# Kernel tuning notes

Hardware: AMD Instinct MI355X
Metric: run time of the kernel (lower is better)

## Reference

```python
import jax, jax.numpy as jnp
import numpy as np


def conv2d(x, w, pad, groups=1):
    # x: [B,Cin,H,W], w: [Cout,Cin/groups,K,K]
    return jax.lax.conv_general_dilated(
        x, w, (1, 1), [(pad, pad), (pad, pad)],
        dimension_numbers=('NCHW', 'OIHW', 'NCHW'),
        feature_group_count=groups)


def setup_inputs() -> dict:
    key = jax.random.key(0)
    ks = jax.random.split(key, 24)
    B, C, H, W = 16, 512, 32, 128          # batch, encoder_dim, feature map
    Da, Ds, De, Dm = 512, 256, 256, 1024   # att_dim, state_dim, embed_dim, mem_dim
    V, Dmerge = 1000, 512
    K, P = 11, 5
    Din = De + C + Dm                       # GRU input dim = 1792
    s = 0.02
    rn = lambda k, shp, sc=1.0: jax.random.normal(k, shp, jnp.float32) * sc
    return {
        'encode': rn(ks[0], (B, C, H, W)),
        'encode_pro': rn(ks[1], (B, Da, H, W)),
        'encode_mask': jnp.ones((B, 1, H, W), jnp.float32),
        'state': rn(ks[2], (B, Ds)),
        'pre_weight': jax.random.uniform(ks[3], (B, 1, H, W), jnp.float32),
        'cum_weight': jax.random.uniform(ks[4], (B, 1, H, W), jnp.float32),
        'context': rn(ks[5], (B, C)),
        'cond_mem': rn(ks[6], (B, Dm)),
        'cond_weight': jax.random.uniform(ks[7], (B, 2, H, W), jnp.float32),
        'label_id': jax.random.randint(ks[8], (B,), 0, V),
        # ImageAttention params (all bias-free per source)
        'w_wt': rn(ks[9], (Da, 1, K, K), s),
        'w_cwt': rn(ks[10], (Da, 1, K, K), s),
        'w_condwt': rn(ks[11], (2 * Da, 1, K, K), s),   # groups=2
        'w_energy': rn(ks[12], (Da,), s),               # 1x1 conv -> vector
        'w_state': rn(ks[13], (Da, Ds), s),
        'w_ctx': rn(ks[14], (Da, C), s),
        'w_cond': rn(ks[15], (Da, Dm), s),
        # GRU params
        'w_i2s': rn(ks[16], (Ds, Din), s), 'b_i2s': jnp.zeros((Ds,), jnp.float32),
        'w_i2g': rn(ks[17], (2 * Ds, Din), s), 'b_i2g': jnp.zeros((2 * Ds,), jnp.float32),
        'w_s2g': rn(ks[18], (2 * Ds, Ds), s),
        'w_h2h': rn(ks[19], (Ds, Ds), s),
        # Readout params
        'embed_table': rn(ks[20], (V, De), s),
        'w_l1': rn(ks[21], (Dmerge, De + Ds + C), s), 'b_l1': jnp.zeros((Dmerge,), jnp.float32),
        'w_l2': rn(ks[22], (V, Dmerge), s), 'b_l2': jnp.zeros((V,), jnp.float32),
    }


def reference(encode, encode_pro, encode_mask, state, pre_weight, cum_weight,
              context, cond_mem, cond_weight, label_id, w_wt, w_cwt, w_condwt,
              w_energy, w_state, w_ctx, w_cond, w_i2s, b_i2s, w_i2g, b_i2g,
              w_s2g, w_h2h, embed_table, w_l1, b_l1, w_l2, b_l2):
    P = (w_wt.shape[-1] - 1) // 2
    Da = w_energy.shape[0]
    B, C, H, W = encode.shape
    # --- ImageAttention ---
    t_pre = conv2d(pre_weight, w_wt, P)           # [B,Da,H,W]
    t_cum = conv2d(cum_weight, w_cwt, P)          # [B,Da,H,W]
    t_cw = conv2d(cond_weight, w_condwt, P, groups=2)
    t_cw = t_cw.reshape(B, 2, Da, H, W).sum(1)    # [B,Da,H,W]
    st = state @ w_state.T + context @ w_ctx.T + cond_mem @ w_cond.T  # [B,Da]
    concat_info = jnp.tanh(st[:, :, None, None] + t_pre + t_cum + t_cw + encode_pro)
    energies = jnp.einsum('bchw,c->bhw', concat_info, w_energy)
    energies = energies + (encode_mask[:, 0] - 1.0) * 1e8
    att = jax.nn.softmax(energies.reshape(B, H * W), axis=1)
    new_weight = att.reshape(B, 1, H, W)
    new_cum_weight = cum_weight + new_weight
    ctx = jnp.einsum('bchw,bhw->bc', encode, new_weight[:, 0])  # [B,C]
    # --- GRU transition (data = [embed, ctx, cond_mem]) ---
    embed = embed_table[label_id]
    data = jnp.concatenate([embed, ctx, cond_mem], axis=1)
    gate = data @ w_i2g.T + b_i2g + state @ w_s2g.T
    Ds = state.shape[1]
    update_g = jax.nn.sigmoid(gate[:, :Ds])
    reset_g = jax.nn.sigmoid(gate[:, Ds:])
    state_hat = jnp.tanh(data @ w_i2s.T + b_i2s + (state * reset_g) @ w_h2h.T)
    new_state = update_g * state_hat + (1.0 - update_g) * state
    # --- Readout.step ---
    merged = jnp.concatenate([embed, new_state, ctx], axis=1)
    hid = jax.nn.relu(merged @ w_l1.T + b_l1)
    readout = hid @ w_l2.T + b_l2                  # [B,V]
    return readout
```

## Files before the change

### kernel.cpp

```cpp
#include <hip/hip_runtime.h>
#include <math.h>

typedef unsigned short u16;
typedef __bf16 bf16x8 __attribute__((ext_vector_type(8)));
typedef float f32x4 __attribute__((ext_vector_type(4)));

__device__ u16   g_A_pack[16 * 512 * 32];
__device__ float g_st[16 * 512];
__device__ float g_eraw[16 * 4096];
__device__ float g_energ[16 * 4096];
__device__ float g_data[16 * 1792];
__device__ float g_merged[16 * 1024];
__device__ float g_update[16 * 256];
__device__ float g_reset[16 * 256];
__device__ float g_i2s[16 * 256];
__device__ float g_hid[16 * 512];

__device__ __forceinline__ u16 f2bf(float f) {
    unsigned u = __float_as_uint(f);
    u = (u + 0x7FFFu + ((u >> 16) & 1u)) >> 16;
    return (u16)u;
}
__device__ __forceinline__ float bf2f(u16 u) {
    return __uint_as_float(((unsigned)u) << 16);
}
__device__ __forceinline__ float fast_tanh(float x) {
    return 1.0f - 2.0f / (__expf(2.0f * x) + 1.0f);
}
__device__ __forceinline__ float sigmoidf_(float x) {
    return 1.0f / (1.0f + __expf(-x));
}

__global__ void k_pre(const float* __restrict__ w_wt, const float* __restrict__ w_cwt,
                      const float* __restrict__ w_condwt, const float* __restrict__ state,
                      const float* __restrict__ context, const float* __restrict__ cond_mem,
                      const float* __restrict__ w_state, const float* __restrict__ w_ctx,
                      const float* __restrict__ w_cond, const int* __restrict__ label,
                      const float* __restrict__ embed_table) {
    int bid = blockIdx.x;
    if (bid < 1024) {
        int idx = bid * 256 + threadIdx.x;
        int d = idx >> 9, k = idx & 511;
        float f = 0.f;
        if (k < 484) {
            int c = k / 121, rem = k % 121;
            if (c == 0)      f = w_wt[d * 121 + rem];
            else if (c == 1) f = w_cwt[d * 121 + rem];
            else if (c == 2) f = w_condwt[d * 121 + rem];
            else             f = w_condwt[(512 + d) * 121 + rem];
        }
        int ks = k >> 5, kl = k & 31;
        g_A_pack[(ks * 512 + d) * 32 + kl] = f2bf(f);
    } else if (bid < 3072) {
        int wid = ((bid - 1024) * 256 + threadIdx.x) >> 6;
        int lane = threadIdx.x & 63;
        if (wid >= 16 * 512) return;
        int b = wid >> 9, d = wid & 511;
        float acc = 0.f;
        for (int k = lane; k < 256; k += 64)  acc += state[b * 256 + k]    * w_state[d * 256 + k];
        for (int k = lane; k < 512; k += 64)  acc += context[b * 512 + k]  * w_ctx[d * 512 + k];
        for (int k = lane; k < 1024; k += 64) acc += cond_mem[b * 1024 + k] * w_cond[d * 1024 + k];
        for (int off = 32; off; off >>= 1) acc += __shfl_down(acc, off, 64);
        if (lane == 0) g_st[b * 512 + d] = acc;
    } else {
        int b = bid - 3072, tid = threadIdx.x;
        int lbl = label[b];
        float ev = embed_table[lbl * 256 + tid];
        g_data[b * 1792 + tid] = ev;
        g_merged[b * 1024 + tid] = ev;
        for (int k = tid; k < 1024; k += 256)
            g_data[b * 1792 + 768 + k] = cond_mem[b * 1024 + k];
    }
}

__global__ __launch_bounds__(512, 4) void k_conv_energy(
    const float* __restrict__ pre_w, const float* __restrict__ cum_w, const float* __restrict__ cond_w,
    const float* __restrict__ encode_pro, const float* __restrict__ w_energy)
{
    __shared__ __align__(16) u16 src[4][11][76];
    __shared__ __align__(16) u16 bchunk[64][40];
    __shared__ __align__(16) u16 epro_l[512 * 68];

    const int blk = blockIdx.x;
    const int pxh = blk & 1;
    const int h = (blk >> 1) & 31;
    const int b = blk >> 6;
    const int px0 = pxh * 64;

    const int tid = threadIdx.x;
    const int lane = tid & 63, wv = tid >> 6;
    const int lr = lane & 15, lg = lane >> 4;

    const float* epbase = encode_pro + (size_t)b * 512 * 4096 + h * 128 + px0;

    float4 ep[4];
#pragma unroll
    for (int i = 0; i < 4; ++i) {
        int o = i * 2048 + tid * 4;
        int r = o >> 6, c = o & 63;
        ep[i] = *reinterpret_cast<const float4*>(&epbase[(size_t)r * 4096 + c]);
    }

#pragma unroll
    for (int it = 0; it < 7; ++it) {
        int t = tid + it * 512;
        if (t < 4 * 11 * 76) {
            int c = t / (11 * 76);
            int rem = t % (11 * 76);
            int i = rem / 76, x = rem % 76;
            int row = h + i - 5, w = px0 - 5 + x;
            u16 v = 0;
            if (x < 74 && row >= 0 && row < 32 && w >= 0 && w < 128) {
                const float* img = (c == 0) ? pre_w + b * 4096
                                 : (c == 1) ? cum_w + b * 4096
                                 : (c == 2) ? cond_w + b * 8192
                                            : cond_w + b * 8192 + 4096;
                v = f2bf(img[row * 128 + w]);
            }
            src[c][i][x] = v;
        }
    }
    __syncthreads();

    const int kl = tid & 31;
    const int n0 = tid >> 5;
#define BUILD(KS)                                                               \
    {                                                                           \
        int kg = (KS) * 32 + kl;                                                \
        int c = 0, i = 0, jj = 0;                                               \
        bool ok = (kg < 484);                                                   \
        if (ok) { c = kg / 121; int r2 = kg % 121; i = r2 / 11; jj = r2 % 11; } \
        _Pragma("unroll")                                                       \
        for (int rep = 0; rep < 4; ++rep) {                                     \
            int n = n0 + rep * 16;                                              \
            bchunk[n][kl] = ok ? src[c][i][n + jj] : (u16)0;                    \
        }                                                                       \
    }

    f32x4 acc[4][4];
#pragma unroll
    for (int mt = 0; mt < 4; ++mt)
#pragma unroll
        for (int nt = 0; nt < 4; ++nt) {
            f32x4 z = {0.f, 0.f, 0.f, 0.f};
            acc[mt][nt] = z;
        }

    BUILD(0);
    __syncthreads();

#pragma unroll
    for (int ks = 0; ks < 16; ++ks) {
        {
            int o = ks * 2048 + tid * 4;
            int r = o >> 6, c = o & 63;
            float4 v = ep[ks & 3];
            ushort4 s;
            s.x = f2bf(v.x); s.y = f2bf(v.y); s.z = f2bf(v.z); s.w = f2bf(v.w);
            *reinterpret_cast<ushort4*>(&epro_l[r * 68 + c]) = s;
            if (ks < 12) {
                int o2 = (ks + 4) * 2048 + tid * 4;
                int r2 = o2 >> 6, c2 = o2 & 63;
                ep[ks & 3] = *reinterpret_cast<const float4*>(&epbase[(size_t)r2 * 4096 + c2]);
            }
        }

        bf16x8 afr[4];
#pragma unroll
        for (int mt = 0; mt < 4; ++mt) {
            int d = wv * 64 + mt * 16 + lr;
            afr[mt] = *reinterpret_cast<const bf16x8*>(&g_A_pack[(ks * 512 + d) * 32 + lg * 8]);
        }
        bf16x8 bfr[4];
#pragma unroll
        for (int nt = 0; nt < 4; ++nt)
            bfr[nt] = *reinterpret_cast<const bf16x8*>(&bchunk[nt * 16 + lr][lg * 8]);

#pragma unroll
        for (int mt = 0; mt < 4; ++mt)
#pragma unroll
            for (int nt = 0; nt < 4; ++nt)
                acc[mt][nt] = __builtin_amdgcn_mfma_f32_16x16x32_bf16(afr[mt], bfr[nt], acc[mt][nt], 0, 0, 0);
        __syncthreads();
        if (ks < 15) {
            BUILD(ks + 1);
            __syncthreads();
        }
    }
#undef BUILD

    float e[4] = {0.f, 0.f, 0.f, 0.f};
#pragma unroll
    for (int mt = 0; mt < 4; ++mt) {
#pragma unroll
        for (int r = 0; r < 4; ++r) {
            int d = wv * 64 + mt * 16 + lg * 4 + r;
            float stv = g_st[b * 512 + d];
            float wev = w_energy[d];
#pragma unroll
            for (int nt = 0; nt < 4; ++nt) {
                int px = nt * 16 + lr;
                float val = stv + acc[mt][nt][r] + bf2f(epro_l[d * 68 + px]);
                e[nt] += wev * fast_tanh(val);
            }
        }
    }

    float* ered = reinterpret_cast<float*>(&bchunk[0][0]);
    __syncthreads();
#pragma unroll
    for (int nt = 0; nt < 4; ++nt) {
        float v = e[nt];
        v += __shfl_xor(v, 16, 64);
        v += __shfl_xor(v, 32, 64);
        if (lane < 16) ered[wv * 64 + nt * 16 + lane] = v;
    }
    __syncthreads();
    if (tid < 64) {
        float v = 0.f;
#pragma unroll
        for (int w = 0; w < 8; ++w) v += ered[w * 64 + tid];
        g_eraw[b * 4096 + h * 128 + px0 + tid] = v;
    }
}

__global__ void k_softmax(const float* __restrict__ encode_mask) {
    __shared__ float red[256];
    int b = blockIdx.x, tid = threadIdx.x;
    float v[16];
    float mx = -1e30f;
#pragma unroll
    for (int i = 0; i < 16; ++i) {
        int idx = b * 4096 + tid + i * 256;
        float ev = g_eraw[idx] + (encode_mask[idx] - 1.0f) * 1e8f;
        v[i] = ev; mx = fmaxf(mx, ev);
    }
    red[tid] = mx; __syncthreads();
    for (int s = 128; s; s >>= 1) { if (tid < s) red[tid] = fmaxf(red[tid], red[tid + s]); __syncthreads(); }
    mx = red[0]; __syncthreads();
    float sum = 0.f;
#pragma unroll
    for (int i = 0; i < 16; ++i) { v[i] = __expf(v[i] - mx); sum += v[i]; }
    red[tid] = sum; __syncthreads();
    for (int s = 128; s; s >>= 1) { if (tid < s) red[tid] += red[tid + s]; __syncthreads(); }
    float inv = 1.0f / red[0];
#pragma unroll
    for (int i = 0; i < 16; ++i) g_energ[b * 4096 + tid + i * 256] = v[i] * inv;
}

__global__ void k_ctx(const float* __restrict__ encode) {
    int wid = (blockIdx.x * blockDim.x + threadIdx.x) >> 6;
    int lane = threadIdx.x & 63;
    if (wid >= 16 * 512) return;
    int b = wid >> 9, c = wid & 511;
    const float* e = encode + (size_t)wid * 4096;
    const float* a = g_energ + b * 4096;
    float acc = 0.f;
#pragma unroll
    for (int it = 0; it < 16; ++it) {
        int base = it * 256 + lane * 4;
        float4 ev = *reinterpret_cast<const float4*>(&e[base]);
        float4 av = *reinterpret_cast<const float4*>(&a[base]);
        acc += ev.x * av.x + ev.y * av.y + ev.z * av.z + ev.w * av.w;
    }
    for (int off = 32; off; off >>= 1) acc += __shfl_down(acc, off, 64);
    if (lane == 0) { g_data[b * 1792 + 256 + c] = acc; g_merged[b * 1024 + 512 + c] = acc; }
}

__global__ void k_e1(const float* __restrict__ state,
                     const float* __restrict__ w_i2g, const float* __restrict__ b_i2g,
                     const float* __restrict__ w_s2g, const float* __restrict__ w_i2s,
                     const float* __restrict__ b_i2s) {
    int wid = (blockIdx.x * blockDim.x + threadIdx.x) >> 6;
    int lane = threadIdx.x & 63;
    if (wid >= 16 * 768) return;
    int b = wid / 768, o = wid % 768;
    const float* dt = g_data + b * 1792;
    float acc = 0.f;
    if (o < 512) {
        const float* wr = w_i2g + o * 1792;
        for (int k = lane; k < 1792; k += 64) acc += dt[k] * wr[k];
        const float* wsg = w_s2g + o * 256;
        for (int k = lane; k < 256; k += 64) acc += state[b * 256 + k] * wsg[k];
    } else {
        const float* wr = w_i2s + (o - 512) * 1792;
        for (int k = lane; k < 1792; k += 64) acc += dt[k] * wr[k];
    }
    for (int off = 32; off; off >>= 1) acc += __shfl_down(acc, off, 64);
    if (lane == 0) {
        if (o < 256)       g_update[b * 256 + o]        = sigmoidf_(acc + b_i2g[o]);
        else if (o < 512)  g_reset[b * 256 + (o - 256)] = sigmoidf_(acc + b_i2g[o]);
        else               g_i2s[b * 256 + (o - 512)]   = acc + b_i2s[o - 512];
    }
}

__global__ void k_e2(const float* __restrict__ state, const float* __restrict__ w_h2h) {
    int wid = (blockIdx.x * blockDim.x + threadIdx.x) >> 6;
    int lane = threadIdx.x & 63;
    if (wid >= 16 * 256) return;
    int b = wid >> 8, d = wid & 255;
    const float* wr = w_h2h + d * 256;
    float acc = 0.f;
    for (int k = lane; k < 256; k += 64)
        acc += state[b * 256 + k] * g_reset[b * 256 + k] * wr[k];
    for (int off = 32; off; off >>= 1) acc += __shfl_down(acc, off, 64);
    if (lane == 0) {
        float sh = fast_tanh(g_i2s[b * 256 + d] + acc);
        float u = g_update[b * 256 + d];
        g_merged[b * 1024 + 256 + d] = u * sh + (1.f - u) * state[b * 256 + d];
    }
}

__global__ void k_e3(const float* __restrict__ w_l1, const float* __restrict__ b_l1) {
    int wid = (blockIdx.x * blockDim.x + threadIdx.x) >> 6;
    int lane = threadIdx.x & 63;
    if (wid >= 16 * 512) return;
    int b = wid >> 9, m = wid & 511;
    const float* mg = g_merged + b * 1024;
    const float* wr = w_l1 + m * 1024;
    float acc = 0.f;
    for (int k = lane; k < 1024; k += 64) acc += mg[k] * wr[k];
    for (int off = 32; off; off >>= 1) acc += __shfl_down(acc, off, 64);
    if (lane == 0) g_hid[b * 512 + m] = fmaxf(acc + b_l1[m], 0.f);
}

__global__ void k_e4(const float* __restrict__ w_l2, const float* __restrict__ b_l2,
                     float* __restrict__ out) {
    int wid = (blockIdx.x * blockDim.x + threadIdx.x) >> 6;
    int lane = threadIdx.x & 63;
    if (wid >= 16 * 1000) return;
    int b = wid / 1000, v = wid % 1000;
    const float* hd = g_hid + b * 512;
    const float* wr = w_l2 + v * 512;
    float acc = 0.f;
    for (int k = lane; k < 512; k += 64) acc += hd[k] * wr[k];
    for (int off = 32; off; off >>= 1) acc += __shfl_down(acc, off, 64);
    if (lane == 0) out[b * 1000 + v] = acc + b_l2[v];
}

extern "C" void kernel_launch(void* const* d_in, const int* in_sizes, int n_in,
                              void* d_out, int out_size, void* d_ws, size_t ws_size,
                              hipStream_t stream) {
    static const int EXP[28] = {
        33554432, 33554432, 65536, 4096, 65536, 65536, 8192, 16384, 131072, 16,
        61952, 61952, 123904, 512, 131072, 262144, 524288, 458752, 256, 917504,
        512, 131072, 65536, 256000, 524288, 512, 512000, 1000};
    if (n_in != 28) return;
    for (int i = 0; i < 28; ++i)
        if (in_sizes[i] != EXP[i]) return;

    const float* encode      = (const float*)d_in[0];
    const float* encode_pro  = (const float*)d_in[1];
    const float* encode_mask = (const float*)d_in[2];
    const float* state       = (const float*)d_in[3];
    const float* pre_weight  = (const float*)d_in[4];
    const float* cum_weight  = (const float*)d_in[5];
    const float* context     = (const float*)d_in[6];
    const float* cond_mem    = (const float*)d_in[7];
    const float* cond_weight = (const float*)d_in[8];
    const int*   label_id    = (const int*)d_in[9];
    const float* w_wt     = (const float*)d_in[10];
    const float* w_cwt    = (const float*)d_in[11];
    const float* w_condwt = (const float*)d_in[12];
    const float* w_energy = (const float*)d_in[13];
    const float* w_state  = (const float*)d_in[14];
    const float* w_ctx    = (const float*)d_in[15];
    const float* w_cond   = (const float*)d_in[16];
    const float* w_i2s    = (const float*)d_in[17];
    const float* b_i2s    = (const float*)d_in[18];
    const float* w_i2g    = (const float*)d_in[19];
    const float* b_i2g    = (const float*)d_in[20];
    const float* w_s2g    = (const float*)d_in[21];
    const float* w_h2h    = (const float*)d_in[22];
    const float* embed_t  = (const float*)d_in[23];
    const float* w_l1     = (const float*)d_in[24];
    const float* b_l1     = (const float*)d_in[25];
    const float* w_l2     = (const float*)d_in[26];
    const float* b_l2     = (const float*)d_in[27];
    float* out = (float*)d_out;
    (void)d_ws; (void)ws_size;

    k_pre<<<3088, 256, 0, stream>>>(w_wt, w_cwt, w_condwt, state, context, cond_mem,
                                    w_state, w_ctx, w_cond, label_id, embed_t);
    k_conv_energy<<<1024, 512, 0, stream>>>(pre_weight, cum_weight, cond_weight,
                                            encode_pro, w_energy);
    k_softmax<<<16, 256, 0, stream>>>(encode_mask);
    k_ctx<<<2048, 256, 0, stream>>>(encode);
    k_e1<<<3072, 256, 0, stream>>>(state, w_i2g, b_i2g, w_s2g, w_i2s, b_i2s);
    k_e2<<<1024, 256, 0, stream>>>(state, w_h2h);
    k_e3<<<2048, 256, 0, stream>>>(w_l1, b_l1);
    k_e4<<<4000, 256, 0, stream>>>(w_l2, b_l2, out);
}
```

Baseline: 198.4 us.

## Halve encode_pro LDS staging and split epilogue into two passes for occupancy

Shrinks the encode_pro shared-memory buffer to 256 channels and stages it in two halves: the first half is loaded up front, and the second is loaded after the first four waves finish their tanh epilogue. It also drops the register-resident prefetch that overlapped encode_pro loads with the MFMA loop, and raises the launch-bounds occupancy hint from 4 to 6. The goal is lower LDS and register usage so more blocks fit per CU. In exchange, encode_pro global loads no longer overlap the MFMA work, and the epilogue becomes serialized, with half the waves idle in each pass.

```diff
diff --git a/kernel.cpp b/kernel.cpp
--- a/kernel.cpp
+++ b/kernel.cpp
@@ -73,13 +73,13 @@
     }
 }
 
-__global__ __launch_bounds__(512, 4) void k_conv_energy(
+__global__ __launch_bounds__(512, 6) void k_conv_energy(
     const float* __restrict__ pre_w, const float* __restrict__ cum_w, const float* __restrict__ cond_w,
     const float* __restrict__ encode_pro, const float* __restrict__ w_energy)
 {
     __shared__ __align__(16) u16 src[4][11][76];
     __shared__ __align__(16) u16 bchunk[64][40];
-    __shared__ __align__(16) u16 epro_l[512 * 68];
+    __shared__ __align__(16) u16 epro_l[256 * 68];
 
     const int blk = blockIdx.x;
     const int pxh = blk & 1;
@@ -93,12 +93,14 @@
 
     const float* epbase = encode_pro + (size_t)b * 512 * 4096 + h * 128 + px0;
 
-    float4 ep[4];
-#pragma unroll
-    for (int i = 0; i < 4; ++i) {
+#pragma unroll
+    for (int i = 0; i < 8; ++i) {
         int o = i * 2048 + tid * 4;
         int r = o >> 6, c = o & 63;
-        ep[i] = *reinterpret_cast<const float4*>(&epbase[(size_t)r * 4096 + c]);
+        float4 v = *reinterpret_cast<const float4*>(&epbase[(size_t)r * 4096 + c]);
+        ushort4 s;
+        s.x = f2bf(v.x); s.y = f2bf(v.y); s.z = f2bf(v.z); s.w = f2bf(v.w);
+        *reinterpret_cast<ushort4*>(&epro_l[r * 68 + c]) = s;
     }
 
 #pragma unroll
@@ -149,22 +151,7 @@
     BUILD(0);
     __syncthreads();
 
-#pragma unroll
     for (int ks = 0; ks < 16; ++ks) {
-        {
-            int o = ks * 2048 + tid * 4;
-            int r = o >> 6, c = o & 63;
-            float4 v = ep[ks & 3];
-            ushort4 s;
-            s.x = f2bf(v.x); s.y = f2bf(v.y); s.z = f2bf(v.z); s.w = f2bf(v.w);
-            *reinterpret_cast<ushort4*>(&epro_l[r * 68 + c]) = s;
-            if (ks < 12) {
-                int o2 = (ks + 4) * 2048 + tid * 4;
-                int r2 = o2 >> 6, c2 = o2 & 63;
-                ep[ks & 3] = *reinterpret_cast<const float4*>(&epbase[(size_t)r2 * 4096 + c2]);
-            }
-        }
-
         bf16x8 afr[4];
 #pragma unroll
         for (int mt = 0; mt < 4; ++mt) {
@@ -190,18 +177,50 @@
 #undef BUILD
 
     float e[4] = {0.f, 0.f, 0.f, 0.f};
-#pragma unroll
-    for (int mt = 0; mt < 4; ++mt) {
-#pragma unroll
-        for (int r = 0; r < 4; ++r) {
-            int d = wv * 64 + mt * 16 + lg * 4 + r;
-            float stv = g_st[b * 512 + d];
-            float wev = w_energy[d];
-#pragma unroll
-            for (int nt = 0; nt < 4; ++nt) {
-                int px = nt * 16 + lr;
-                float val = stv + acc[mt][nt][r] + bf2f(epro_l[d * 68 + px]);
-                e[nt] += wev * fast_tanh(val);
+    if (wv < 4) {
+#pragma unroll
+        for (int mt = 0; mt < 4; ++mt) {
+#pragma unroll
+            for (int r = 0; r < 4; ++r) {
+                int d = wv * 64 + mt * 16 + lg * 4 + r;
+                float stv = g_st[b * 512 + d];
+                float wev = w_energy[d];
+#pragma unroll
+                for (int nt = 0; nt < 4; ++nt) {
+                    int px = nt * 16 + lr;
+                    float val = stv + acc[mt][nt][r] + bf2f(epro_l[d * 68 + px]);
+                    e[nt] += wev * fast_tanh(val);
+                }
+            }
+        }
+    }
+    __syncthreads();
+
+#pragma unroll
+    for (int i = 0; i < 8; ++i) {
+        int o = i * 2048 + tid * 4;
+        int r = o >> 6, c = o & 63;
+        float4 v = *reinterpret_cast<const float4*>(&epbase[(size_t)(256 + r) * 4096 + c]);
+        ushort4 s;
+        s.x = f2bf(v.x); s.y = f2bf(v.y); s.z = f2bf(v.z); s.w = f2bf(v.w);
+        *reinterpret_cast<ushort4*>(&epro_l[r * 68 + c]) = s;
+    }
+    __syncthreads();
+
+    if (wv >= 4) {
+#pragma unroll
+        for (int mt = 0; mt < 4; ++mt) {
+#pragma unroll
+            for (int r = 0; r < 4; ++r) {
+                int d = wv * 64 + mt * 16 + lg * 4 + r;
+                float stv = g_st[b * 512 + d];
+                float wev = w_energy[d];
+#pragma unroll
+                for (int nt = 0; nt < 4; ++nt) {
+                    int px = nt * 16 + lr;
+                    float val = stv + acc[mt][nt][r] + bf2f(epro_l[(d - 256) * 68 + px]);
+                    e[nt] += wev * fast_tanh(val);
+                }
             }
         }
     }
```

After: 378.6 us. 90.8% more time.
